# Optimization experiments

Hardware: AMD Instinct MI355X
Metric: run time of the kernel (lower is better)

The kernel has to match this reference:

```python
import jax, jax.numpy as jnp
import numpy as np

D_MODEL = 1024
N_HEADS = 16
HEAD_DIM = D_MODEL // N_HEADS


def setup_inputs() -> dict:
    key = jax.random.key(0)
    ks = jax.random.split(key, 5)
    B, T = 4, 2048
    scale = 0.02
    x = jax.random.normal(ks[0], (B, T, D_MODEL), dtype=jnp.float32)
    W_qkv = jax.random.normal(ks[1], (D_MODEL, 3 * D_MODEL), dtype=jnp.float32) * scale
    b_qkv = jnp.zeros((3 * D_MODEL,), dtype=jnp.float32)
    W_out = jax.random.normal(ks[2], (D_MODEL, D_MODEL), dtype=jnp.float32) * scale
    b_out = jnp.zeros((D_MODEL,), dtype=jnp.float32)
    return {"x": x, "W_qkv": W_qkv, "b_qkv": b_qkv, "W_out": W_out, "b_out": b_out}


def reference(x, W_qkv, b_qkv, W_out, b_out):
    B, T, C = x.shape
    H, Dh = N_HEADS, HEAD_DIM
    qkv = x @ W_qkv + b_qkv                      # (B,T,3C)
    q, k, v = jnp.split(qkv, 3, axis=-1)
    # (B,T,C) -> (B,H,T,Dh)
    q = q.reshape(B, T, H, Dh).transpose(0, 2, 1, 3)
    k = k.reshape(B, T, H, Dh).transpose(0, 2, 1, 3)
    v = v.reshape(B, T, H, Dh).transpose(0, 2, 1, 3)
    scores = jnp.einsum("bhqd,bhkd->bhqk", q, k) / jnp.sqrt(jnp.float32(Dh))
    causal = jnp.tril(jnp.ones((T, T), dtype=bool))  # True = keep
    scores = jnp.where(causal, scores, jnp.float32(-jnp.inf))
    attn = jax.nn.softmax(scores, axis=-1)
    out = jnp.einsum("bhqk,bhkd->bhqd", attn, v)  # (B,H,T,Dh)
    concat = out.transpose(0, 2, 1, 3).reshape(B, T, C)
    return concat @ W_out + b_out
```

## Files before the change

### kernel.cpp

```cpp
#include <hip/hip_runtime.h>
#include <math.h>

typedef __attribute__((ext_vector_type(8))) short bf16x8;
typedef __attribute__((ext_vector_type(4))) float f32x4;
typedef unsigned short u16;
typedef unsigned int u32;

#define TSEQ 2048
#define NH   16
#define DH   64
#define CDIM 1024
#define SCLQ 0.18033688011112042f

__device__ __forceinline__ u16 f2bf(float f) {
    union { float f; u32 u; } v; v.f = f;
    u32 r = v.u + 0x7fffu + ((v.u >> 16) & 1u);
    return (u16)(r >> 16);
}

__device__ __forceinline__ u32 cvtpk(float lo, float hi) {
    u32 r;
    asm("v_cvt_pk_bf16_f32 %0, %1, %2" : "=v"(r) : "v"(lo), "v"(hi));
    return r;
}

__device__ __forceinline__ float max3f(float a, float b, float c) {
    return fmaxf(fmaxf(a, b), c);
}

__device__ __forceinline__ void gl_lds16(const void* g, void* l) {
    __builtin_amdgcn_global_load_lds(
        (const __attribute__((address_space(1))) u32*)g,
        (__attribute__((address_space(3))) u32*)l, 16, 0, 0);
}

#define MFMA16(a, b, c) __builtin_amdgcn_mfma_f32_16x16x32_bf16(a, b, c, 0, 0, 0)

#define WAITV(n) do { asm volatile("s_waitcnt vmcnt(" #n ")" ::: "memory"); } while (0)
#define WAITL()  do { asm volatile("s_waitcnt lgkmcnt(0)" ::: "memory"); } while (0)
#define BARC()   do { __builtin_amdgcn_s_barrier(); __builtin_amdgcn_sched_barrier(0); } while (0)

__global__ __launch_bounds__(256) void prep(
    const float* __restrict__ x, const float* __restrict__ Wq,
    const float* __restrict__ Wo,
    u16* __restrict__ xb, u16* __restrict__ Wqt, u16* __restrict__ Wot) {
    const int bid = blockIdx.x, tid = threadIdx.x;
    if (bid < 4096) {
        int i = (bid * 256 + tid) * 8;
        float4 a = *(const float4*)(x + i);
        float4 b = *(const float4*)(x + i + 4);
        u16 o[8] = {f2bf(a.x), f2bf(a.y), f2bf(a.z), f2bf(a.w),
                    f2bf(b.x), f2bf(b.y), f2bf(b.z), f2bf(b.w)};
        *(uint4*)(xb + i) = *(const uint4*)o;
        return;
    }
    __shared__ float tile[32][33];
    const float* Wf; u16* Wt; int K, N, n0, k0;
    if (bid < 4096 + 3072) {
        int b2 = bid - 4096;
        Wf = Wq; Wt = Wqt; K = 1024; N = 3072;
        n0 = (b2 % 96) * 32; k0 = (b2 / 96) * 32;
    } else {
        int b2 = bid - 7168;
        Wf = Wo; Wt = Wot; K = 1024; N = 1024;
        n0 = (b2 & 31) * 32; k0 = (b2 >> 5) * 32;
    }
    int tx = tid & 31, ty = tid >> 5;
#pragma unroll
    for (int r = 0; r < 4; r++)
        tile[ty + r * 8][tx] = Wf[(k0 + ty + r * 8) * N + n0 + tx];
    __syncthreads();
#pragma unroll
    for (int r = 0; r < 4; r++)
        Wt[(n0 + ty + r * 8) * K + k0 + tx] = f2bf(tile[tx][ty + r * 8]);
}

template <int EPI>
__global__ __launch_bounds__(512, 1) void gemm256(
    const u16* __restrict__ A, const u16* __restrict__ Bt,
    const float* __restrict__ bias,
    u16* __restrict__ O0, u16* __restrict__ O1, u16* __restrict__ O2,
    float* __restrict__ Of) {
    __shared__ u16 lA[2][2][128 * 64];
    __shared__ u16 lB[2][2][128 * 64];

    const int tid = threadIdx.x;
    const int lane = tid & 63, w = tid >> 6;
    const int l15 = lane & 15, l4 = lane >> 4;
    const int wm = w >> 2, wn = w & 3;
    const int nwg = gridDim.x;
    const int wg = (blockIdx.x & 7) * (nwg >> 3) + (blockIdx.x >> 3);
    const int mi = wg & 31, ni = wg >> 5;
    const size_t mb = (size_t)mi * 256, nb = (size_t)ni * 256;
    const int KD = 1024;

    auto stA = [&](int t, int half, int buf) {
        int kb = (t & 15) * 64;
#pragma unroll
        for (int s = 0; s < 2; s++) {
            int i2 = s * 512 + tid;
            int row = i2 >> 3, g = i2 & 7;
            int gsw = g ^ (row & 7);
            gl_lds16(A + (mb + half * 128 + row) * KD + kb + gsw * 8,
                     &lA[buf][half][i2 * 8]);
        }
    };
    auto stB = [&](int t, int half, int buf) {
        int kb = (t & 15) * 64;
#pragma unroll
        for (int s = 0; s < 2; s++) {
            int i2 = s * 512 + tid;
            int row = i2 >> 3, g = i2 & 7;
            int gsw = g ^ (row & 7);
            gl_lds16(Bt + (nb + half * 128 + row) * KD + kb + gsw * 8,
                     &lB[buf][half][i2 * 8]);
        }
    };

    f32x4 zero = {0.f, 0.f, 0.f, 0.f};
    f32x4 acc[8][4];
#pragma unroll
    for (int i = 0; i < 8; i++)
#pragma unroll
        for (int j = 0; j < 4; j++) acc[i][j] = zero;

    const int hB = wn >> 1, rBb = (wn & 1) * 64;

    stB(0, 0, 0); stA(0, 0, 0); stB(0, 1, 0); stA(0, 1, 0);
    stB(1, 0, 1); stA(1, 0, 1); stB(1, 1, 1);
    WAITV(6);
    BARC();

    bf16x8 a8[4][2], bA[2][2], bB[2][2];

    for (int t = 0; t < 16; t++) {
        const int p = t & 1, q = p ^ 1;
#pragma unroll
        for (int fm = 0; fm < 4; fm++) {
            int r = fm * 16 + l15;
            const u16* base = &lA[p][wm][r * 64];
            a8[fm][0] = *(const bf16x8*)(base + ((l4) ^ (r & 7)) * 8);
            a8[fm][1] = *(const bf16x8*)(base + ((4 + l4) ^ (r & 7)) * 8);
        }
#pragma unroll
        for (int fn = 0; fn < 2; fn++) {
            int r = rBb + fn * 16 + l15;
            const u16* base = &lB[p][hB][r * 64];
            bA[fn][0] = *(const bf16x8*)(base + ((l4) ^ (r & 7)) * 8);
            bA[fn][1] = *(const bf16x8*)(base + ((4 + l4) ^ (r & 7)) * 8);
        }
        stA(t + 1, 1, q);
        __builtin_amdgcn_s_barrier();
        WAITL();
        __builtin_amdgcn_s_setprio(1);
#pragma unroll
        for (int fm = 0; fm < 4; fm++)
#pragma unroll
            for (int fn = 0; fn < 2; fn++) {
                acc[fm][fn] = MFMA16(a8[fm][0], bA[fn][0], acc[fm][fn]);
                acc[fm][fn] = MFMA16(a8[fm][1], bA[fn][1], acc[fm][fn]);
            }
        __builtin_amdgcn_s_setprio(0);
        BARC();
#pragma unroll
        for (int fn = 0; fn < 2; fn++) {
            int r = rBb + (fn + 2) * 16 + l15;
            const u16* base = &lB[p][hB][r * 64];
            bB[fn][0] = *(const bf16x8*)(base + ((l4) ^ (r & 7)) * 8);
            bB[fn][1] = *(const bf16x8*)(base + ((4 + l4) ^ (r & 7)) * 8);
        }
        __builtin_amdgcn_s_barrier();
        WAITL();
        __builtin_amdgcn_s_setprio(1);
#pragma unroll
        for (int fm = 0; fm < 4; fm++)
#pragma unroll
            for (int fn = 0; fn < 2; fn++) {
                acc[fm][fn + 2] = MFMA16(a8[fm][0], bB[fn][0], acc[fm][fn + 2]);
                acc[fm][fn + 2] = MFMA16(a8[fm][1], bB[fn][1], acc[fm][fn + 2]);
            }
        __builtin_amdgcn_s_setprio(0);
        BARC();
#pragma unroll
        for (int fm = 0; fm < 4; fm++) {
            int r = (fm + 4) * 16 + l15;
            const u16* base = &lA[p][wm][r * 64];
            a8[fm][0] = *(const bf16x8*)(base + ((l4) ^ (r & 7)) * 8);
            a8[fm][1] = *(const bf16x8*)(base + ((4 + l4) ^ (r & 7)) * 8);
        }
        stB(t + 2, 0, p);
        __builtin_amdgcn_s_barrier();
        WAITL();
        __builtin_amdgcn_s_setprio(1);
#pragma unroll
        for (int fm = 0; fm < 4; fm++)
#pragma unroll
            for (int fn = 0; fn < 2; fn++) {
                acc[fm + 4][fn + 2] = MFMA16(a8[fm][0], bB[fn][0], acc[fm + 4][fn + 2]);
                acc[fm + 4][fn + 2] = MFMA16(a8[fm][1], bB[fn][1], acc[fm + 4][fn + 2]);
            }
        __builtin_amdgcn_s_setprio(0);
        BARC();
        stA(t + 2, 0, p); stB(t + 2, 1, p);
        __builtin_amdgcn_s_barrier();
        __builtin_amdgcn_s_setprio(1);
#pragma unroll
        for (int fm = 0; fm < 4; fm++)
#pragma unroll
            for (int fn = 0; fn < 2; fn++) {
                acc[fm + 4][fn] = MFMA16(a8[fm][0], bA[fn][0], acc[fm + 4][fn]);
                acc[fm + 4][fn] = MFMA16(a8[fm][1], bA[fn][1], acc[fm + 4][fn]);
            }
        __builtin_amdgcn_s_setprio(0);
        WAITV(6);
        BARC();
    }
    WAITV(0);

#pragma unroll
    for (int fm = 0; fm < 8; fm++)
#pragma unroll
        for (int fn = 0; fn < 4; fn++) {
            int n = (int)nb + wn * 64 + fn * 16 + l15;
            int m0 = (int)mb + wm * 128 + fm * 16 + l4 * 4;
            float bz = bias[n];
            if (EPI == 0) {
#pragma unroll
                for (int i = 0; i < 4; i++)
                    Of[(size_t)(m0 + i) * CDIM + n] = acc[fm][fn][i] + bz;
            } else {
                int which = n >> 10, hh = (n >> 6) & 15, d = n & 63;
                int b = m0 >> 11, t0 = m0 & 2047;
                if (which == 0) {
#pragma unroll
                    for (int i = 0; i < 4; i++)
                        O0[((b * NH + hh) * TSEQ + t0 + i) * DH + d] =
                            f2bf((acc[fm][fn][i] + bz) * SCLQ);
                } else if (which == 1) {
#pragma unroll
                    for (int i = 0; i < 4; i++)
                        O1[((b * NH + hh) * TSEQ + t0 + i) * DH + d] =
                            f2bf(acc[fm][fn][i] + bz);
                } else {
                    u16 ov[4];
#pragma unroll
                    for (int i = 0; i < 4; i++) ov[i] = f2bf(acc[fm][fn][i] + bz);
                    *(uint2*)&O2[((b * NH + hh) * DH + d) * TSEQ + t0] =
                        *(const uint2*)ov;
                }
            }
        }
}

__global__ __launch_bounds__(256, 4) void attn_mfma(
    const u16* __restrict__ Q, const u16* __restrict__ K,
    const u16* __restrict__ Vt, u16* __restrict__ Oc) {
    __shared__ u16 Kl[2][4096];
    __shared__ u16 Vl[2][4096];
    __shared__ u16 Pl[4096];

    const int tid = threadIdx.x;
    const int lane = tid & 63, w = tid >> 6;
    const int l15 = lane & 15, l4 = lane >> 4;
    const int bh = blockIdx.x & 63;
    const int pair = blockIdx.x >> 6;
    const int qt0 = pair, qt1 = 31 - pair;
    const int NT = qt1 + 1;

    const u16* Qb = Q + bh * TSEQ * DH;
    const u16* Kb = K + bh * TSEQ * DH;
    const u16* Vb = Vt + bh * DH * TSEQ;

    auto STAGE = [&](int kt, int p) {
#pragma unroll
        for (int r = 0; r < 2; r++) {
            int idx = r * 256 + tid;
            int row = idx >> 3, h = idx & 7;
            int hs = h ^ (row & 7);
            gl_lds16(Kb + (kt * 64 + row) * DH + hs * 8, &Kl[p][idx * 8]);
            gl_lds16(Vb + row * TSEQ + kt * 64 + hs * 8, &Vl[p][idx * 8]);
        }
    };

    const int qrow0 = qt0 * 64 + w * 16 + l15;
    const int qrow1 = qt1 * 64 + w * 16 + l15;
    bf16x8 q0a, q0b, q1a, q1b;
    {
        const u16* qp = Qb + qrow0 * DH + l4 * 8;
        q0a = *(const bf16x8*)(qp);
        q0b = *(const bf16x8*)(qp + 32);
    }
    {
        const u16* qp = Qb + qrow1 * DH + l4 * 8;
        q1a = *(const bf16x8*)(qp);
        q1b = *(const bf16x8*)(qp + 32);
    }

    f32x4 zero = {0.f, 0.f, 0.f, 0.f};
    f32x4 o0[4], o1[4];
    float m0 = -INFINITY, l0 = 0.f, m1 = -INFINITY, l1 = 0.f;
#pragma unroll
    for (int i = 0; i < 4; i++) { o0[i] = zero; o1[i] = zero; }

    auto SMPV = [&](f32x4* s, float& m_r, float& l_r, f32x4* oacc,
                    int q_row, bool domask, int kt, int p) {
        if (domask) {
#pragma unroll
            for (int c = 0; c < 4; c++)
#pragma unroll
                for (int i = 0; i < 4; i++) {
                    int kg = kt * 64 + c * 16 + l4 * 4 + i;
                    if (kg > q_row) s[c][i] = -INFINITY;
                }
        }
        float a0 = max3f(s[0][0], s[0][1], s[0][2]);
        float a1 = max3f(s[0][3], s[1][0], s[1][1]);
        float a2 = max3f(s[1][2], s[1][3], s[2][0]);
        float a3 = max3f(s[2][1], s[2][2], s[2][3]);
        float a4 = max3f(s[3][0], s[3][1], s[3][2]);
        float mx = max3f(max3f(a0, a1, a2), fmaxf(a3, a4), s[3][3]);
        mx = fmaxf(mx, __shfl_xor(mx, 16));
        mx = fmaxf(mx, __shfl_xor(mx, 32));
        if (!__all(mx <= m_r)) {
            float mnew = fmaxf(m_r, mx);
            float corr = __builtin_amdgcn_exp2f(m_r - mnew);
            l_r *= corr;
            float cr[4];
#pragma unroll
            for (int r = 0; r < 4; r++) cr[r] = __shfl(corr, l4 * 4 + r);
#pragma unroll
            for (int dg = 0; dg < 4; dg++)
#pragma unroll
                for (int r = 0; r < 4; r++) oacc[dg][r] *= cr[r];
            m_r = mnew;
        }
        float pv[16];
#pragma unroll
        for (int c = 0; c < 4; c++)
#pragma unroll
            for (int i = 0; i < 4; i++)
                pv[c * 4 + i] = __builtin_amdgcn_exp2f(s[c][i] - m_r);
        float t0 = (pv[0] + pv[1]) + (pv[2] + pv[3]);
        float t1 = (pv[4] + pv[5]) + (pv[6] + pv[7]);
        float t2 = (pv[8] + pv[9]) + (pv[10] + pv[11]);
        float t3 = (pv[12] + pv[13]) + (pv[14] + pv[15]);
        float rs = (t0 + t1) + (t2 + t3);
        rs += __shfl_xor(rs, 16);
        rs += __shfl_xor(rs, 32);
        l_r += rs;

#pragma unroll
        for (int c = 0; c < 4; c++) {
            uint2 pr;
            pr.x = cvtpk(pv[c * 4 + 0], pv[c * 4 + 1]);
            pr.y = cvtpk(pv[c * 4 + 2], pv[c * 4 + 3]);
            int g = (c << 1) + (l4 >> 1);
            int gp = g ^ (l15 & 7);
            *(uint2*)&Pl[w * 1024 + l15 * 64 + gp * 8 + ((l4 & 1) << 2)] = pr;
        }

        __builtin_amdgcn_s_setprio(1);
#pragma unroll
        for (int kk = 0; kk < 2; kk++) {
            int grp = ((kk << 2) + l4) ^ (l15 & 7);
            bf16x8 pf = *(const bf16x8*)&Pl[w * 1024 + l15 * 64 + grp * 8];
#pragma unroll
            for (int dg = 0; dg < 4; dg++) {
                int drow = (dg << 4) + l15;
                bf16x8 vf = *(const bf16x8*)(&Vl[p][drow * 64 + grp * 8]);
                oacc[dg] = MFMA16(pf, vf, oacc[dg]);
            }
        }
        __builtin_amdgcn_s_setprio(0);
    };

    STAGE(0, 0);

    for (int kt = 0; kt < NT; kt++) {
        const int p = kt & 1;
        __syncthreads();
        if (kt + 1 < NT) {
            STAGE(kt + 1, p ^ 1);
            asm volatile("s_waitcnt vmcnt(4)" ::: "memory");
        } else {
            asm volatile("s_waitcnt vmcnt(0)" ::: "memory");
        }
        __syncthreads();

        const bool act0 = (kt <= qt0);

        f32x4 s1[4], s0[4];
        __builtin_amdgcn_s_setprio(1);
#pragma unroll
        for (int c = 0; c < 4; c++) {
            int trow = c * 16 + l15;
            int swz = l15 & 7;
            bf16x8 kf0 = *(const bf16x8*)(&Kl[p][trow * 64 + (l4 ^ swz) * 8]);
            bf16x8 kf1 = *(const bf16x8*)(&Kl[p][trow * 64 + ((4 + l4) ^ swz) * 8]);
            f32x4 a = zero;
            a = MFMA16(kf0, q1a, a);
            a = MFMA16(kf1, q1b, a);
            s1[c] = a;
            if (act0) {
                f32x4 b = zero;
                b = MFMA16(kf0, q0a, b);
                b = MFMA16(kf1, q0b, b);
                s0[c] = b;
            }
        }
        __builtin_amdgcn_s_setprio(0);

        SMPV(s1, m1, l1, o1, qrow1, kt == qt1, kt, p);
        if (act0) {
            asm volatile("s_waitcnt lgkmcnt(0)" ::: "memory");
            SMPV(s0, m0, l0, o0, qrow0, kt == qt0, kt, p);
        }
    }

    const int b = bh >> 4, hh = bh & 15;
    {
        float inv[4];
#pragma unroll
        for (int r = 0; r < 4; r++) inv[r] = 1.0f / __shfl(l0, l4 * 4 + r);
        int tb = qt0 * 64 + w * 16 + l4 * 4;
#pragma unroll
        for (int r = 0; r < 4; r++)
#pragma unroll
            for (int dg = 0; dg < 4; dg++)
                Oc[(b * TSEQ + tb + r) * CDIM + hh * DH + (dg << 4) + l15] =
                    f2bf(o0[dg][r] * inv[r]);
    }
    {
        float inv[4];
#pragma unroll
        for (int r = 0; r < 4; r++) inv[r] = 1.0f / __shfl(l1, l4 * 4 + r);
        int tb = qt1 * 64 + w * 16 + l4 * 4;
#pragma unroll
        for (int r = 0; r < 4; r++)
#pragma unroll
            for (int dg = 0; dg < 4; dg++)
                Oc[(b * TSEQ + tb + r) * CDIM + hh * DH + (dg << 4) + l15] =
                    f2bf(o1[dg][r] * inv[r]);
    }
}

extern "C" void kernel_launch(void* const* d_in, const int* in_sizes, int n_in,
                              void* d_out, int out_size, void* d_ws, size_t ws_size,
                              hipStream_t stream) {
    const float* x     = (const float*)d_in[0];
    const float* W_qkv = (const float*)d_in[1];
    const float* b_qkv = (const float*)d_in[2];
    const float* W_out = (const float*)d_in[3];
    const float* b_out = (const float*)d_in[4];
    float* out = (float*)d_out;

    u16* xb  = (u16*)d_ws;
    u16* Wqt = xb  + 8388608;
    u16* Wot = Wqt + 3145728;
    u16* Qw  = Wot + 1048576;
    u16* Kw  = Qw  + 8388608;
    u16* Vtw = Kw  + 8388608;
    u16* Ocw = Vtw + 8388608;

    prep<<<8192, 256, 0, stream>>>(x, W_qkv, W_out, xb, Wqt, Wot);
    gemm256<1><<<384, 512, 0, stream>>>(xb, Wqt, b_qkv, Qw, Kw, Vtw, nullptr);
    attn_mfma<<<1024, 256, 0, stream>>>(Qw, Kw, Vtw, Ocw);
    gemm256<0><<<128, 512, 0, stream>>>(Ocw, Wot, b_out, nullptr, nullptr, nullptr, out);
}
```

Measured before the change: 289.3 us.

## Replace 256x256 GEMM with 128x256 triple-buffered K32 pipeline for higher occupancy

After: 263.3 us. 9.0% less time.

```diff
diff --git a/kernel.cpp b/kernel.cpp
--- a/kernel.cpp
+++ b/kernel.cpp
@@ -37,8 +37,11 @@
 #define MFMA16(a, b, c) __builtin_amdgcn_mfma_f32_16x16x32_bf16(a, b, c, 0, 0, 0)
 
 #define WAITV(n) do { asm volatile("s_waitcnt vmcnt(" #n ")" ::: "memory"); } while (0)
-#define WAITL()  do { asm volatile("s_waitcnt lgkmcnt(0)" ::: "memory"); } while (0)
+#define WAITL()  do { asm volatile("s_waitcnt lgkmcnt(0)" ::: "memory"); \
+                      __builtin_amdgcn_sched_barrier(0); } while (0)
 #define BARC()   do { __builtin_amdgcn_s_barrier(); __builtin_amdgcn_sched_barrier(0); } while (0)
+
+__device__ __forceinline__ int swz4(int r) { return (r & 3) ^ ((r >> 2) & 3); }
 
 __global__ __launch_bounds__(256) void prep(
     const float* __restrict__ x, const float* __restrict__ Wq,
@@ -76,13 +79,13 @@
 }
 
 template <int EPI>
-__global__ __launch_bounds__(512, 1) void gemm256(
+__global__ __launch_bounds__(512, 4) void gemm_r3(
     const u16* __restrict__ A, const u16* __restrict__ Bt,
     const float* __restrict__ bias,
     u16* __restrict__ O0, u16* __restrict__ O1, u16* __restrict__ O2,
     float* __restrict__ Of) {
-    __shared__ u16 lA[2][2][128 * 64];
-    __shared__ u16 lB[2][2][128 * 64];
+    __shared__ u16 lA[3][128 * 32];
+    __shared__ u16 lB[3][256 * 32];
 
     const int tid = threadIdx.x;
     const int lane = tid & 63, w = tid >> 6;
@@ -90,139 +93,80 @@
     const int wm = w >> 2, wn = w & 3;
     const int nwg = gridDim.x;
     const int wg = (blockIdx.x & 7) * (nwg >> 3) + (blockIdx.x >> 3);
-    const int mi = wg & 31, ni = wg >> 5;
-    const size_t mb = (size_t)mi * 256, nb = (size_t)ni * 256;
+    const int mi = wg & 63, ni = wg >> 6;
+    const size_t mb = (size_t)mi * 128, nb = (size_t)ni * 256;
     const int KD = 1024;
 
-    auto stA = [&](int t, int half, int buf) {
-        int kb = (t & 15) * 64;
+    const int srowA = tid >> 2, sgA = tid & 3;
+    const int sgswA = sgA ^ swz4(srowA);
+    auto stA = [&](int ts, int buf) {
+        gl_lds16(A + (mb + srowA) * KD + ts * 32 + sgswA * 8,
+                 &lA[buf][tid * 8]);
+    };
+    auto stB = [&](int ts, int buf) {
 #pragma unroll
         for (int s = 0; s < 2; s++) {
-            int i2 = s * 512 + tid;
-            int row = i2 >> 3, g = i2 & 7;
-            int gsw = g ^ (row & 7);
-            gl_lds16(A + (mb + half * 128 + row) * KD + kb + gsw * 8,
-                     &lA[buf][half][i2 * 8]);
+            int idx = s * 512 + tid;
+            int row = idx >> 2, g = idx & 3;
+            gl_lds16(Bt + (nb + row) * KD + ts * 32 + (g ^ swz4(row)) * 8,
+                     &lB[buf][idx * 8]);
         }
     };
-    auto stB = [&](int t, int half, int buf) {
-        int kb = (t & 15) * 64;
-#pragma unroll
-        for (int s = 0; s < 2; s++) {
-            int i2 = s * 512 + tid;
-            int row = i2 >> 3, g = i2 & 7;
-            int gsw = g ^ (row & 7);
-            gl_lds16(Bt + (nb + half * 128 + row) * KD + kb + gsw * 8,
-                     &lB[buf][half][i2 * 8]);
-        }
-    };
 
     f32x4 zero = {0.f, 0.f, 0.f, 0.f};
-    f32x4 acc[8][4];
-#pragma unroll
-    for (int i = 0; i < 8; i++)
+    f32x4 acc[4][4];
+#pragma unroll
+    for (int i = 0; i < 4; i++)
 #pragma unroll
         for (int j = 0; j < 4; j++) acc[i][j] = zero;
 
-    const int hB = wn >> 1, rBb = (wn & 1) * 64;
-
-    stB(0, 0, 0); stA(0, 0, 0); stB(0, 1, 0); stA(0, 1, 0);
-    stB(1, 0, 1); stA(1, 0, 1); stB(1, 1, 1);
-    WAITV(6);
+    int aOff[4], bOff[4];
+#pragma unroll
+    for (int f = 0; f < 4; f++) {
+        int ra = wm * 64 + f * 16 + l15;
+        aOff[f] = (ra << 5) + (l4 ^ swz4(ra)) * 8;
+        int rb = wn * 64 + f * 16 + l15;
+        bOff[f] = (rb << 5) + (l4 ^ swz4(rb)) * 8;
+    }
+
+    stA(0, 0); stB(0, 0);
+    stA(1, 1); stB(1, 1);
+    WAITV(3);
     BARC();
 
-    bf16x8 a8[4][2], bA[2][2], bB[2][2];
-
-    for (int t = 0; t < 16; t++) {
-        const int p = t & 1, q = p ^ 1;
-#pragma unroll
-        for (int fm = 0; fm < 4; fm++) {
-            int r = fm * 16 + l15;
-            const u16* base = &lA[p][wm][r * 64];
-            a8[fm][0] = *(const bf16x8*)(base + ((l4) ^ (r & 7)) * 8);
-            a8[fm][1] = *(const bf16x8*)(base + ((4 + l4) ^ (r & 7)) * 8);
-        }
-#pragma unroll
-        for (int fn = 0; fn < 2; fn++) {
-            int r = rBb + fn * 16 + l15;
-            const u16* base = &lB[p][hB][r * 64];
-            bA[fn][0] = *(const bf16x8*)(base + ((l4) ^ (r & 7)) * 8);
-            bA[fn][1] = *(const bf16x8*)(base + ((4 + l4) ^ (r & 7)) * 8);
-        }
-        stA(t + 1, 1, q);
-        __builtin_amdgcn_s_barrier();
+#pragma unroll
+    for (int t = 0; t < 32; t++) {
+        const int buf = t % 3;
+        const int bs = (t + 2) % 3;
+        const int ts = (t + 2 > 31) ? 31 : t + 2;
+        stA(ts, bs); stB(ts, bs);
+
+        bf16x8 a8[4], b8[4];
+#pragma unroll
+        for (int f = 0; f < 4; f++) a8[f] = *(const bf16x8*)(&lA[buf][aOff[f]]);
+#pragma unroll
+        for (int f = 0; f < 4; f++) b8[f] = *(const bf16x8*)(&lB[buf][bOff[f]]);
+
+        WAITV(3);
         WAITL();
+        BARC();
+
         __builtin_amdgcn_s_setprio(1);
 #pragma unroll
         for (int fm = 0; fm < 4; fm++)
 #pragma unroll
-            for (int fn = 0; fn < 2; fn++) {
-                acc[fm][fn] = MFMA16(a8[fm][0], bA[fn][0], acc[fm][fn]);
-                acc[fm][fn] = MFMA16(a8[fm][1], bA[fn][1], acc[fm][fn]);
-            }
+            for (int fn = 0; fn < 4; fn++)
+                acc[fm][fn] = MFMA16(a8[fm], b8[fn], acc[fm][fn]);
         __builtin_amdgcn_s_setprio(0);
-        BARC();
-#pragma unroll
-        for (int fn = 0; fn < 2; fn++) {
-            int r = rBb + (fn + 2) * 16 + l15;
-            const u16* base = &lB[p][hB][r * 64];
-            bB[fn][0] = *(const bf16x8*)(base + ((l4) ^ (r & 7)) * 8);
-            bB[fn][1] = *(const bf16x8*)(base + ((4 + l4) ^ (r & 7)) * 8);
-        }
-        __builtin_amdgcn_s_barrier();
-        WAITL();
-        __builtin_amdgcn_s_setprio(1);
-#pragma unroll
-        for (int fm = 0; fm < 4; fm++)
-#pragma unroll
-            for (int fn = 0; fn < 2; fn++) {
-                acc[fm][fn + 2] = MFMA16(a8[fm][0], bB[fn][0], acc[fm][fn + 2]);
-                acc[fm][fn + 2] = MFMA16(a8[fm][1], bB[fn][1], acc[fm][fn + 2]);
-            }
-        __builtin_amdgcn_s_setprio(0);
-        BARC();
-#pragma unroll
-        for (int fm = 0; fm < 4; fm++) {
-            int r = (fm + 4) * 16 + l15;
-            const u16* base = &lA[p][wm][r * 64];
-            a8[fm][0] = *(const bf16x8*)(base + ((l4) ^ (r & 7)) * 8);
-            a8[fm][1] = *(const bf16x8*)(base + ((4 + l4) ^ (r & 7)) * 8);
-        }
-        stB(t + 2, 0, p);
-        __builtin_amdgcn_s_barrier();
-        WAITL();
-        __builtin_amdgcn_s_setprio(1);
-#pragma unroll
-        for (int fm = 0; fm < 4; fm++)
-#pragma unroll
-            for (int fn = 0; fn < 2; fn++) {
-                acc[fm + 4][fn + 2] = MFMA16(a8[fm][0], bB[fn][0], acc[fm + 4][fn + 2]);
-                acc[fm + 4][fn + 2] = MFMA16(a8[fm][1], bB[fn][1], acc[fm + 4][fn + 2]);
-            }
-        __builtin_amdgcn_s_setprio(0);
-        BARC();
-        stA(t + 2, 0, p); stB(t + 2, 1, p);
-        __builtin_amdgcn_s_barrier();
-        __builtin_amdgcn_s_setprio(1);
-#pragma unroll
-        for (int fm = 0; fm < 4; fm++)
-#pragma unroll
-            for (int fn = 0; fn < 2; fn++) {
-                acc[fm + 4][fn] = MFMA16(a8[fm][0], bA[fn][0], acc[fm + 4][fn]);
-                acc[fm + 4][fn] = MFMA16(a8[fm][1], bA[fn][1], acc[fm + 4][fn]);
-            }
-        __builtin_amdgcn_s_setprio(0);
-        WAITV(6);
-        BARC();
     }
     WAITV(0);
 
 #pragma unroll
-    for (int fm = 0; fm < 8; fm++)
+    for (int fm = 0; fm < 4; fm++)
 #pragma unroll
         for (int fn = 0; fn < 4; fn++) {
             int n = (int)nb + wn * 64 + fn * 16 + l15;
-            int m0 = (int)mb + wm * 128 + fm * 16 + l4 * 4;
+            int m0 = (int)mb + wm * 64 + fm * 16 + l4 * 4;
             float bz = bias[n];
             if (EPI == 0) {
 #pragma unroll
@@ -463,7 +407,7 @@
     u16* Ocw = Vtw + 8388608;
 
     prep<<<8192, 256, 0, stream>>>(x, W_qkv, W_out, xb, Wqt, Wot);
-    gemm256<1><<<384, 512, 0, stream>>>(xb, Wqt, b_qkv, Qw, Kw, Vtw, nullptr);
+    gemm_r3<1><<<768, 512, 0, stream>>>(xb, Wqt, b_qkv, Qw, Kw, Vtw, nullptr);
     attn_mfma<<<1024, 256, 0, stream>>>(Qw, Kw, Vtw, Ocw);
-    gemm256<0><<<128, 512, 0, stream>>>(Ocw, Wot, b_out, nullptr, nullptr, nullptr, out);
-}
+    gemm_r3<0><<<256, 512, 0, stream>>>(Ocw, Wot, b_out, nullptr, nullptr, nullptr, out);
+}
```
